# Kernel optimization log

Hardware: AMD Instinct MI355X
Metric: run time of the kernel (lower is better)

The kernel has to match this reference:

```python
import jax, jax.numpy as jnp
import numpy as np

B, N, F_IN, H, HID = 2, 1024, 128, 4, 32  # batch, nodes, in_feat, heads, hidden per head


def setup_inputs() -> dict:
    key = jax.random.key(0)
    k1, k2, k3, k4 = jax.random.split(key, 4)
    node_feat = jax.random.normal(k1, (B, N, F_IN), dtype=jnp.float32)
    adj_mtx = jax.random.randint(k2, (B, N, N), 0, 2, dtype=jnp.int32)  # 0/1 adjacency
    # xavier_normal init for params
    W = jax.random.normal(k3, (F_IN, H * HID), dtype=jnp.float32) * np.sqrt(2.0 / (F_IN + H * HID))
    Wa = jax.random.normal(k4, (H, HID), dtype=jnp.float32) * np.sqrt(2.0 / (H + HID))
    return {"node_feat": node_feat, "adj_mtx": adj_mtx, "W": W, "Wa": Wa}


def reference(node_feat, adj_mtx, W, Wa):
    b, n, _ = node_feat.shape
    h, hid = Wa.shape
    # projected features: (B, H, N, hid)
    x = (node_feat @ W).reshape(b, n, h, hid).transpose(0, 2, 1, 3)
    # GATv2 additive scores: leaky_relu(x_i + x_j) . Wa  -> (B, H, N, N)
    s = jax.nn.leaky_relu(x[:, :, :, None, :] + x[:, :, None, :, :], negative_slope=0.2)
    e = jnp.einsum('bhijk,hk->bhij', s, Wa)
    # mask non-edges, softmax over neighbors j
    e = jnp.where(adj_mtx[:, None, :, :] > 0, e, -jnp.inf)
    att = jax.nn.softmax(e, axis=-1)
    # aggregate values: (B, H, N, hid)
    xp = jnp.einsum('bhij,bhjd->bhid', att, x)
    # concat heads -> (B, N, H*hid)
    return xp.transpose(0, 2, 1, 3).reshape(b, n, h * hid)
```

## Files before the change

### kernel.cpp

```cpp
#include <hip/hip_runtime.h>
#include <math.h>

#define BB 2
#define NN 1024
#define HH 4
#define F_IN 128
#define HID 32
#define TJ 64
#define NT 16
#define CT 8

#define LOG2E 1.44269504f

typedef unsigned long long u64;
typedef unsigned int u32;
typedef _Float16 f16;
typedef _Float16 h2    __attribute__((ext_vector_type(2)));
typedef _Float16 f16x4 __attribute__((ext_vector_type(4)));
typedef _Float16 f16x8 __attribute__((ext_vector_type(8)));
typedef float f32x4 __attribute__((ext_vector_type(4)));

#define WS_XH  0
#define WS_D6  524288
#define WS_XT  557056

#if __has_builtin(__builtin_amdgcn_fdot2)
#define FDOT2(a, b, c) __builtin_amdgcn_fdot2((a), (b), (c), false)
#else
static __device__ __forceinline__ float FDOT2(h2 a, h2 b, float c) {
    return fmaf((float)a[0], (float)b[0], fmaf((float)a[1], (float)b[1], c));
}
#endif

template <typename D, typename S>
static __device__ __forceinline__ D bcast(S s) { return __builtin_bit_cast(D, s); }

__global__ __launch_bounds__(128) void gat_proj_kernel(const float* __restrict__ feat,
        const float* __restrict__ W, const float* __restrict__ Wa,
        f16* __restrict__ xh, f16* __restrict__ xt, float* __restrict__ d6) {
    const int RPB = 4;
    int blk = blockIdx.x;
    int b  = blk / (NN / RPB);
    int n0 = (blk % (NN / RPB)) * RPB;
    int t  = threadIdx.x;

    __shared__ float fs[RPB][F_IN];
#pragma unroll
    for (int e = 0; e < RPB; ++e) {
        int idx = e * 128 + t;
        int r = idx >> 7, f = idx & 127;
        fs[r][f] = feat[((size_t)(b*NN + n0 + r))*F_IN + f];
    }
    __syncthreads();

    float acc[RPB];
#pragma unroll
    for (int r = 0; r < RPB; ++r) acc[r] = 0.f;
    for (int f = 0; f < F_IN; ++f) {
        float w = W[f*(HH*HID) + t];
#pragma unroll
        for (int r = 0; r < RPB; ++r) acc[r] = fmaf(fs[r][f], w, acc[r]);
    }

    int h = t >> 5, k = t & 31;
    int bh = b*HH + h;
#pragma unroll
    for (int r = 0; r < RPB; ++r)
        xh[((size_t)bh*NN + n0 + r)*HID + k] = (f16)acc[r];
    {
        f16x4 hv;
#pragma unroll
        for (int r = 0; r < RPB; ++r) hv[r] = (f16)acc[r];
        *(f16x4*)(xt + ((size_t)bh*HID + k)*NN + n0) = hv;
    }
    float w_t = Wa[t];
#pragma unroll
    for (int r = 0; r < RPB; ++r) {
        float p = acc[r] * w_t;
#pragma unroll
        for (int off = 16; off >= 1; off >>= 1) p += __shfl_xor(p, off, 32);
        if (k == 0) d6[(size_t)bh*NN + n0 + r] = 0.6f * LOG2E * p;
    }
}

__device__ __forceinline__ u32 srfl(u32 v) { return __builtin_amdgcn_readfirstlane(v); }

__global__ __launch_bounds__(512) void gat_fused_kernel(const f16* __restrict__ xh,
                                                        const float* __restrict__ d6,
                                                        const int* __restrict__ adj,
                                                        const float* __restrict__ Wa,
                                                        const f16* __restrict__ xt,
                                                        float* __restrict__ out) {
    const int tid = threadIdx.x;
    const int w = __builtin_amdgcn_readfirstlane(tid >> 6);
    const int l = tid & 63;
    const int blk = blockIdx.x;
    const int bh = blk & 7;
    const int i0 = (blk >> 3) << 4;
    const int h = bh & 3, b = bh >> 2;
    const int q4 = w & 3, hf = w >> 2;
    const int ib = i0 + 4*q4;

    const u32* xhu = (const u32*)(xh + (size_t)bh*NN*HID);
    const float* dbh = d6 + (size_t)bh*NN;

    __shared__ __align__(16) f16 Pl[16][1032];
    __shared__ float scr[8][64][9];
    __shared__ float lsp2[2][16];

    u32 wa2[16];
    {
        const float* wap = Wa + h*HID;
#pragma unroll
        for (int q = 0; q < 16; ++q) {
            h2 hw;
            hw[0] = (f16)((0.4f*LOG2E) * wap[2*q]);
            hw[1] = (f16)((0.4f*LOG2E) * wap[2*q+1]);
            wa2[q] = srfl(bcast<u32>(hw));
        }
    }
    u32 xi2[4][16];
    float ci[4];
#pragma unroll
    for (int r = 0; r < 4; ++r) {
        const u32* xr = xhu + (size_t)(ib + r)*16;
#pragma unroll
        for (int q = 0; q < 16; ++q) xi2[r][q] = srfl(xr[q]);
        ci[r] = __uint_as_float(srfl(__float_as_uint(dbh[ib + r]))) - 8.0f;
    }

    const int* adj0 = adj + ((size_t)b*NN + ib + 0)*NN;
    const int* adj1 = adj + ((size_t)b*NN + ib + 1)*NN;
    const int* adj2 = adj + ((size_t)b*NN + ib + 2)*NN;
    const int* adj3 = adj + ((size_t)b*NN + ib + 3)*NN;

    float ls0 = 0.f, ls1 = 0.f, ls2 = 0.f, ls3 = 0.f;

    for (int tt = 0; tt < CT; ++tt) {
        const int j = (hf*CT + tt)*TJ + l;
        u64 m0 = __ballot(adj0[j] > 0);
        u64 m1 = __ballot(adj1[j] > 0);
        u64 m2 = __ballot(adj2[j] > 0);
        u64 m3 = __ballot(adj3[j] > 0);
        float dj = dbh[j];

        const u32* xjp = xhu + (size_t)j*16;
        uint4 xa = *(const uint4*)(xjp);
        uint4 xb = *(const uint4*)(xjp + 4);
        uint4 xc = *(const uint4*)(xjp + 8);
        uint4 xd = *(const uint4*)(xjp + 12);
        u32 xj[16] = {xa.x, xa.y, xa.z, xa.w, xb.x, xb.y, xb.z, xb.w,
                      xc.x, xc.y, xc.z, xc.w, xd.x, xd.y, xd.z, xd.w};

        float s0 = 0.f, s1 = 0.f, s2 = 0.f, s3 = 0.f;
#pragma unroll
        for (int q = 0; q < 16; ++q) {
            h2 xjh = bcast<h2>(xj[q]);
            h2 wq  = bcast<h2>(wa2[q]);
            h2 v; u32 a;
            v = bcast<h2>(xi2[0][q]) + xjh; a = bcast<u32>(v) & 0x7fff7fffu;
            s0 = FDOT2(bcast<h2>(a), wq, s0);
            v = bcast<h2>(xi2[1][q]) + xjh; a = bcast<u32>(v) & 0x7fff7fffu;
            s1 = FDOT2(bcast<h2>(a), wq, s1);
            v = bcast<h2>(xi2[2][q]) + xjh; a = bcast<u32>(v) & 0x7fff7fffu;
            s2 = FDOT2(bcast<h2>(a), wq, s2);
            v = bcast<h2>(xi2[3][q]) + xjh; a = bcast<u32>(v) & 0x7fff7fffu;
            s3 = FDOT2(bcast<h2>(a), wq, s3);
        }
        float p0 = exp2f(ci[0] + dj + s0);
        float p1 = exp2f(ci[1] + dj + s1);
        float p2 = exp2f(ci[2] + dj + s2);
        float p3 = exp2f(ci[3] + dj + s3);
        asm("v_cndmask_b32 %0, 0, %1, %2" : "=v"(p0) : "v"(p0), "s"(m0));
        asm("v_cndmask_b32 %0, 0, %1, %2" : "=v"(p1) : "v"(p1), "s"(m1));
        asm("v_cndmask_b32 %0, 0, %1, %2" : "=v"(p2) : "v"(p2), "s"(m2));
        asm("v_cndmask_b32 %0, 0, %1, %2" : "=v"(p3) : "v"(p3), "s"(m3));
        ls0 += p0; ls1 += p1; ls2 += p2; ls3 += p3;
        Pl[4*q4 + 0][j] = (f16)p0;
        Pl[4*q4 + 1][j] = (f16)p1;
        Pl[4*q4 + 2][j] = (f16)p2;
        Pl[4*q4 + 3][j] = (f16)p3;
    }

#pragma unroll
    for (int off = 32; off >= 1; off >>= 1) {
        ls0 += __shfl_xor(ls0, off, 64);
        ls1 += __shfl_xor(ls1, off, 64);
        ls2 += __shfl_xor(ls2, off, 64);
        ls3 += __shfl_xor(ls3, off, 64);
    }
    if (l == 0) {
        lsp2[hf][4*q4 + 0] = ls0;
        lsp2[hf][4*q4 + 1] = ls1;
        lsp2[hf][4*q4 + 2] = ls2;
        lsp2[hf][4*q4 + 3] = ls3;
    }
    __syncthreads();

    const f16* xtb = xt + (size_t)bh * HID * NN;
    const int lrow = l & 15, lslot = (l >> 4) << 3;

    f32x4 acc0 = {0.f, 0.f, 0.f, 0.f};
    f32x4 acc1 = {0.f, 0.f, 0.f, 0.f};
#pragma unroll
    for (int q = 0; q < 4; ++q) {
        const int joff = (w*4 + q)*32 + lslot;
        f16x8 af = *(const f16x8*)&Pl[lrow][joff];
        f16x8 b0 = *(const f16x8*)(xtb + (size_t)lrow*NN + joff);
        f16x8 b1 = *(const f16x8*)(xtb + (size_t)(16 + lrow)*NN + joff);
        acc0 = __builtin_amdgcn_mfma_f32_16x16x32_f16(af, b0, acc0, 0, 0, 0);
        acc1 = __builtin_amdgcn_mfma_f32_16x16x32_f16(af, b1, acc1, 0, 0, 0);
    }

#pragma unroll
    for (int e = 0; e < 4; ++e) {
        scr[w][l][e]     = acc0[e];
        scr[w][l][4 + e] = acc1[e];
    }
    __syncthreads();

    {
        float s = 0.f;
#pragma unroll
        for (int ww = 0; ww < 8; ++ww) s += scr[ww][l][w];
        const int r = w & 3;
        const int col = ((w >= 4) ? 16 : 0) + lrow;
        const int rloc = ((l >> 4) << 2) + r;
        const int row = i0 + rloc;
        float inv = 1.0f / (lsp2[0][rloc] + lsp2[1][rloc]);
        out[((size_t)(b*NN + row))*(HH*HID) + h*HID + col] = s * inv;
    }
}

extern "C" void kernel_launch(void* const* d_in, const int* in_sizes, int n_in,
                              void* d_out, int out_size, void* d_ws, size_t ws_size,
                              hipStream_t stream) {
    const float* node_feat = (const float*)d_in[0];
    const int*   adj_mtx   = (const int*)d_in[1];
    const float* W         = (const float*)d_in[2];
    const float* Wa        = (const float*)d_in[3];
    float* out = (float*)d_out;

    char* ws = (char*)d_ws;
    f16*   xh_ws = (f16*)(ws + WS_XH);
    float* d6_ws = (float*)(ws + WS_D6);
    f16*   xt_ws = (f16*)(ws + WS_XT);

    hipLaunchKernelGGL(gat_proj_kernel, dim3(BB*NN/4), dim3(128), 0, stream,
                       node_feat, W, Wa, xh_ws, xt_ws, d6_ws);
    hipLaunchKernelGGL(gat_fused_kernel, dim3(8 * (NN/16)), dim3(512), 0, stream,
                       xh_ws, d6_ws, adj_mtx, Wa, xt_ws, out);
}
```

Baseline: 35.79 us.

## Compute P·V with two waves over full j range, drop cross-wave reduction

The aggregation stage used to split the j dimension across all 8 waves and then reduce partial MFMA results through a shared-memory scratch buffer and a second barrier. Now only waves 0 and 1 run, each covering all 32 j-tiles for one 16-column half of the hidden dimension, and write normalized outputs directly. This removes the scratch buffer, one barrier and the reduction pass. In exchange the MFMA chain is serialized on two waves, 32 dependent MFMAs each, while six waves sit idle.

After: 37.29 us. 1.04x slower.

```diff
diff --git a/kernel.cpp b/kernel.cpp
--- a/kernel.cpp
+++ b/kernel.cpp
@@ -105,7 +105,6 @@
     const float* dbh = d6 + (size_t)bh*NN;
 
     __shared__ __align__(16) f16 Pl[16][1032];
-    __shared__ float scr[8][64][9];
     __shared__ float lsp2[2][16];
 
     u32 wa2[16];
@@ -197,38 +196,26 @@
     }
     __syncthreads();
 
-    const f16* xtb = xt + (size_t)bh * HID * NN;
-    const int lrow = l & 15, lslot = (l >> 4) << 3;
-
-    f32x4 acc0 = {0.f, 0.f, 0.f, 0.f};
-    f32x4 acc1 = {0.f, 0.f, 0.f, 0.f};
-#pragma unroll
-    for (int q = 0; q < 4; ++q) {
-        const int joff = (w*4 + q)*32 + lslot;
-        f16x8 af = *(const f16x8*)&Pl[lrow][joff];
-        f16x8 b0 = *(const f16x8*)(xtb + (size_t)lrow*NN + joff);
-        f16x8 b1 = *(const f16x8*)(xtb + (size_t)(16 + lrow)*NN + joff);
-        acc0 = __builtin_amdgcn_mfma_f32_16x16x32_f16(af, b0, acc0, 0, 0, 0);
-        acc1 = __builtin_amdgcn_mfma_f32_16x16x32_f16(af, b1, acc1, 0, 0, 0);
-    }
-
-#pragma unroll
-    for (int e = 0; e < 4; ++e) {
-        scr[w][l][e]     = acc0[e];
-        scr[w][l][4 + e] = acc1[e];
-    }
-    __syncthreads();
-
-    {
-        float s = 0.f;
-#pragma unroll
-        for (int ww = 0; ww < 8; ++ww) s += scr[ww][l][w];
-        const int r = w & 3;
-        const int col = ((w >= 4) ? 16 : 0) + lrow;
-        const int rloc = ((l >> 4) << 2) + r;
-        const int row = i0 + rloc;
-        float inv = 1.0f / (lsp2[0][rloc] + lsp2[1][rloc]);
-        out[((size_t)(b*NN + row))*(HH*HID) + h*HID + col] = s * inv;
+    if (w < 2) {
+        const f16* xtb = xt + (size_t)bh * HID * NN + (size_t)(w * 16) * NN;
+        const int lrow = l & 15, lslot = (l >> 4) << 3;
+
+        f32x4 acc = {0.f, 0.f, 0.f, 0.f};
+#pragma unroll
+        for (int jt = 0; jt < 32; ++jt) {
+            const int joff = jt*32 + lslot;
+            f16x8 af = *(const f16x8*)&Pl[lrow][joff];
+            f16x8 bf = *(const f16x8*)(xtb + (size_t)lrow*NN + joff);
+            acc = __builtin_amdgcn_mfma_f32_16x16x32_f16(af, bf, acc, 0, 0, 0);
+        }
+
+#pragma unroll
+        for (int r = 0; r < 4; ++r) {
+            const int rloc = ((l >> 4) << 2) + r;
+            const int row = i0 + rloc;
+            float inv = 1.0f / (lsp2[0][rloc] + lsp2[1][rloc]);
+            out[((size_t)(b*NN + row))*(HH*HID) + h*HID + w*16 + lrow] = acc[r] * inv;
+        }
     }
 }
 
```
